# Optimization experiments

Measured on AMD Instinct MI355X. Metric: run time of the kernel, lower is better.

## Reference

```python
import jax, jax.numpy as jnp
import numpy as np

HID = 64
NUM_LAYER = 3
N_OBJ = 100000
N_P1, N_P2, N_P3 = 200000, 400000, 200000
NUM_GRAPHS = 256


def _mlp(x, w1, b1, w2, b2):
    # pyg.nn.MLP([in, hid, out], norm=None): Linear -> ReLU -> Linear
    return jnp.dot(jax.nn.relu(jnp.dot(x, w1) + b1), w2) + b2


def _gather(obj, ei):
    # ei: [arity, n_atoms] object index per argument slot
    r, n = ei.shape
    g = jnp.take(obj, ei, axis=0)  # [r, n, HID]
    return jnp.moveaxis(g, 0, 1).reshape(n, r * HID)  # concat per-position embeddings


def _scatter(atom, ei, n_obj):
    # split atom embedding [n, r*HID] into r chunks and scatter-add to objects
    r, n = ei.shape
    chunks = jnp.moveaxis(atom.reshape(n, r, HID), 1, 0).reshape(r * n, HID)
    return jax.ops.segment_sum(chunks, ei.reshape(-1), num_segments=n_obj)


def _lin_init(key, fan_in, fan_out):
    kw, kb = jax.random.split(key)
    w = jax.random.normal(kw, (fan_in, fan_out), jnp.float32) / np.float32(np.sqrt(fan_in))
    b = jax.random.normal(kb, (fan_out,), jnp.float32) * 0.01
    return w, b


def setup_inputs() -> dict:
    key = jax.random.key(0)
    ks = jax.random.split(key, 16)
    inp = {}
    inp["x_obj"] = jnp.zeros((N_OBJ, 1), jnp.float32)
    inp["x_p1"] = jnp.zeros((N_P1, 1), jnp.float32)
    inp["x_p2"] = jnp.zeros((N_P2, 2), jnp.float32)
    inp["x_p3"] = jnp.zeros((N_P3, 3), jnp.float32)
    for i, (name, r) in enumerate([("p1", 1), ("p2", 2), ("p3", 3)]):
        d = HID * r
        w1, b1 = _lin_init(ks[2 * i], d, d)
        w2, b2 = _lin_init(ks[2 * i + 1], d, d)
        inp[f"w_{name}_1"], inp[f"b_{name}_1"] = w1, b1
        inp[f"w_{name}_2"], inp[f"b_{name}_2"] = w2, b2
    inp["w_u1"], inp["b_u1"] = _lin_init(ks[6], 2 * HID, 2 * HID)
    inp["w_u2"], inp["b_u2"] = _lin_init(ks[7], 2 * HID, HID)
    inp["w_r1"], inp["b_r1"] = _lin_init(ks[8], HID, 2 * HID)
    inp["w_r2"], inp["b_r2"] = _lin_init(ks[9], 2 * HID, 1)
    inp["ei_p1"] = jax.random.randint(ks[10], (1, N_P1), 0, N_OBJ, jnp.int32)
    inp["ei_p2"] = jax.random.randint(ks[11], (2, N_P2), 0, N_OBJ, jnp.int32)
    inp["ei_p3"] = jax.random.randint(ks[12], (3, N_P3), 0, N_OBJ, jnp.int32)
    inp["batch_obj"] = jnp.sort(jax.random.randint(ks[13], (N_OBJ,), 0, NUM_GRAPHS, jnp.int32))
    inp["num_graphs"] = NUM_GRAPHS
    return inp


def reference(x_obj, x_p1, x_p2, x_p3,
              w_p1_1, b_p1_1, w_p1_2, b_p1_2,
              w_p2_1, b_p2_1, w_p2_2, b_p2_2,
              w_p3_1, b_p3_1, w_p3_2, b_p3_2,
              w_u1, b_u1, w_u2, b_u2,
              w_r1, b_r1, w_r2, b_r2,
              ei_p1, ei_p2, ei_p3, batch_obj, num_graphs):
    n_obj = x_obj.shape[0]
    # encoding_layer: everything starts at zeros of size [N, F*hidden]
    obj = jnp.zeros((n_obj, x_obj.shape[1] * HID), jnp.float32)
    for _ in range(NUM_LAYER):
        # FanOutMP: gather arg-object embeddings, per-predicate MLP -> atom embeddings
        a1 = _mlp(_gather(obj, ei_p1), w_p1_1, b_p1_1, w_p1_2, b_p1_2)
        a2 = _mlp(_gather(obj, ei_p2), w_p2_1, b_p2_1, w_p2_2, b_p2_2)
        a3 = _mlp(_gather(obj, ei_p3), w_p3_1, b_p3_1, w_p3_2, b_p3_2)
        # FanInMP: split atom emb into arity chunks, scatter-add back to objects
        agg = (_scatter(a1, ei_p1, n_obj) + _scatter(a2, ei_p2, n_obj)
               + _scatter(a3, ei_p3, n_obj))
        # obj_update on cat([old_obj, aggregated])
        obj = _mlp(jnp.concatenate([obj, agg], axis=1), w_u1, b_u1, w_u2, b_u2)
    # global_add_pool + readout
    pooled = jax.ops.segment_sum(obj, batch_obj, num_segments=num_graphs)
    return _mlp(pooled, w_r1, b_r1, w_r2, b_r2).reshape(-1)
```

## Files before the change

### kernel.cpp

```cpp
#include <hip/hip_runtime.h>
#include <hip/hip_fp16.h>

typedef _Float16 h8 __attribute__((ext_vector_type(8)));
typedef float f32x4 __attribute__((ext_vector_type(4)));

__device__ __forceinline__ f32x4 mfma2(h8 ah, h8 bh, h8 bl, f32x4 c) {
    c = __builtin_amdgcn_mfma_f32_16x16x32_f16(ah, bh, c, 0, 0, 0);
    c = __builtin_amdgcn_mfma_f32_16x16x32_f16(ah, bl, c, 0, 0, 0);
    return c;
}

__launch_bounds__(256)
__global__ void setup_k(const float* __restrict__ w_p1_1, const float* __restrict__ w_p1_2,
                        const float* __restrict__ w_p2_1, const float* __restrict__ w_p2_2,
                        const float* __restrict__ w_p3_1, const float* __restrict__ w_p3_2,
                        const float* __restrict__ w_u1, const float* __restrict__ w_u2,
                        _Float16* __restrict__ hb,
                        const float* __restrict__ b_p1_1, const float* __restrict__ b_p1_2,
                        const float* __restrict__ b_p2_1, const float* __restrict__ b_p2_2,
                        const float* __restrict__ b_p3_1, const float* __restrict__ b_p3_2,
                        float* __restrict__ ac,
                        const int* __restrict__ ei1, const int* __restrict__ ei2,
                        const int* __restrict__ ei3, int* __restrict__ counts,
                        int n_obj, int n1, int n2, int n3)
{
    int b = blockIdx.x;
    if (b < 544) {
        const float* src; int K, N, base; size_t off;
        if      (b < 16)  { src = w_p1_1; K = 64;  N = 64;  base = 0;   off = 0;      }
        else if (b < 32)  { src = w_p1_2; K = 64;  N = 64;  base = 16;  off = 8192;   }
        else if (b < 96)  { src = w_p2_1; K = 128; N = 128; base = 32;  off = 16384;  }
        else if (b < 160) { src = w_p2_2; K = 128; N = 128; base = 96;  off = 49152;  }
        else if (b < 304) { src = w_p3_1; K = 192; N = 192; base = 160; off = 81920;  }
        else if (b < 448) { src = w_p3_2; K = 192; N = 192; base = 304; off = 155648; }
        else if (b < 512) { src = w_u1;   K = 128; N = 128; base = 448; off = 229376; }
        else              { src = w_u2;   K = 128; N = 64;  base = 512; off = 262144; }
        int e = (b - base) * 256 + threadIdx.x;
        if (e < K * N) {
            int n = e / K, k = e - n * K;
            float x = src[k * N + n];
            _Float16 h = (_Float16)x;
            hb[off + e] = h;
            hb[off + (size_t)K * N + e] = (_Float16)(x - (float)h);
        }
    } else if (b < 547) {
        int p = b - 544;
        const float *b1, *w2, *b2; int D, off;
        if      (p == 0) { b1 = b_p1_1; w2 = w_p1_2; b2 = b_p1_2; D = 64;  off = 0;   }
        else if (p == 1) { b1 = b_p2_1; w2 = w_p2_2; b2 = b_p2_2; D = 128; off = 64;  }
        else             { b1 = b_p3_1; w2 = w_p3_2; b2 = b_p3_2; D = 192; off = 192; }
        int n = threadIdx.x;
        if (n < D) {
            float s = b2[n];
            for (int k = 0; k < D; ++k) {
                float h = b1[k];
                h = h > 0.f ? h : 0.f;
                s = fmaf(h, w2[k * D + n], s);
            }
            ac[off + n] = s;
        }
    } else {
        int e = (b - 547) * 256 + threadIdx.x;
        int t1 = n1, t2 = n1 + 2 * n2, t3 = t2 + 3 * n3;
        int o, j;
        if (e < t1) { o = ei1[e]; j = 0; }
        else if (e < t2) { int x = e - t1; o = ei2[x]; j = 1 + (x >= n2 ? 1 : 0); }
        else if (e < t3) { int y = e - t2; o = ei3[y]; j = 3 + (y >= n3 ? 1 : 0) + (y >= 2 * n3 ? 1 : 0); }
        else return;
        atomicAdd(&counts[(size_t)j * n_obj + o], 1);
        atomicAdd(&counts[(size_t)6 * n_obj + o], 1);
    }
}

__launch_bounds__(256)
__global__ void scan1_k(const int* __restrict__ deg, int* __restrict__ rowptr,
                        int* __restrict__ bsum, int n)
{
    __shared__ int buf[256];
    int tid = threadIdx.x;
    int base = blockIdx.x * 1024 + tid * 4;
    int v[4];
#pragma unroll
    for (int k = 0; k < 4; ++k) { int i = base + k; v[k] = (i < n) ? deg[i] : 0; }
    int tsum = v[0] + v[1] + v[2] + v[3];
    buf[tid] = tsum;
    __syncthreads();
    for (int off = 1; off < 256; off <<= 1) {
        int t = (tid >= off) ? buf[tid - off] : 0;
        __syncthreads();
        buf[tid] += t;
        __syncthreads();
    }
    int run = buf[tid] - tsum;
#pragma unroll
    for (int k = 0; k < 4; ++k) {
        int i = base + k;
        if (i < n) rowptr[i] = run;
        run += v[k];
    }
    if (tid == 255) bsum[blockIdx.x] = buf[255];
}

__launch_bounds__(256)
__global__ void scan2_k(int* __restrict__ bsum, int* __restrict__ rowptr, int n, int nb)
{
    __shared__ int buf[256];
    int tid = threadIdx.x;
    int v = (tid < nb) ? bsum[tid] : 0;
    buf[tid] = v;
    __syncthreads();
    for (int off = 1; off < 256; off <<= 1) {
        int t = (tid >= off) ? buf[tid - off] : 0;
        __syncthreads();
        buf[tid] += t;
        __syncthreads();
    }
    if (tid < nb) bsum[tid] = buf[tid] - v;
    if (tid == 255) rowptr[n] = buf[255];
}

__launch_bounds__(256)
__global__ void scan3_k(int* __restrict__ rowptr, int* __restrict__ cursor,
                        const int* __restrict__ bsum, int n)
{
    int i = blockIdx.x * 256 + threadIdx.x;
    if (i < n) {
        int r = rowptr[i] + bsum[i >> 10];
        rowptr[i] = r;
        cursor[i] = r;
    }
}

__launch_bounds__(256)
__global__ void fill_k(const int* __restrict__ ei1, const int* __restrict__ ei2,
                       const int* __restrict__ ei3, int* __restrict__ cursor,
                       int* __restrict__ epos, int n1, int n2, int n3)
{
    int e = blockIdx.x * 256 + threadIdx.x;
    int t1 = n1, t2 = n1 + 2 * n2, t3 = t2 + 3 * n3;
    int o;
    if (e < t1) o = ei1[e];
    else if (e < t2) o = ei2[e - t1];
    else if (e < t3) o = ei3[e - t2];
    else return;
    epos[e] = atomicAdd(&cursor[o], 1);
}

__launch_bounds__(256)
__global__ void bcast_k(const int* __restrict__ counts, const float* __restrict__ ac,
                        _Float16* __restrict__ aggh, int n_obj)
{
    __shared__ float ch[384];
    int tid = threadIdx.x;
    for (int i = tid; i < 384; i += 256) ch[i] = ac[i];
    __syncthreads();
    int i = blockIdx.x * 256 + tid;
    int o = i >> 3, q = i & 7;
    if (o < n_obj) {
        float c[6];
#pragma unroll
        for (int j = 0; j < 6; ++j) c[j] = (float)counts[(size_t)j * n_obj + o];
        h8 v;
#pragma unroll
        for (int comp = 0; comp < 8; ++comp) {
            int col = 8 * q + comp;
            float s = 0.f;
#pragma unroll
            for (int j = 0; j < 6; ++j) s = fmaf(c[j], ch[j * 64 + col], s);
            v[comp] = (_Float16)s;
        }
        *(h8*)(aggh + (size_t)o * 64 + 8 * q) = v;
    }
}

__device__ __forceinline__ void update_tail(
    _Float16* __restrict__ Ah, _Float16* __restrict__ objh,
    const _Float16* __restrict__ W1h, const _Float16* __restrict__ W1l,
    const float* __restrict__ B1,
    const _Float16* __restrict__ W2h, const _Float16* __restrict__ W2l,
    const float* __restrict__ B2,
    int n_obj, int a_base, int last, float* __restrict__ aggf)
{
    constexpr int LDA = 136;
    const int tid = threadIdx.x;
    const int wave = tid >> 6, lane = tid & 63;
    const int r = lane & 15, g = lane >> 4;

    f32x4 z = {0.f, 0.f, 0.f, 0.f};
    f32x4 acc[4][2];
#pragma unroll
    for (int rt = 0; rt < 4; ++rt) { acc[rt][0] = z; acc[rt][1] = z; }
    {
        h8 bh[2][2], bl[2][2];
#pragma unroll
        for (int t = 0; t < 2; ++t) {
            size_t wo = (size_t)((wave * 2 + t) * 16 + r) * 128 + g * 8;
            bh[0][t] = *(const h8*)(W1h + wo);
            bl[0][t] = *(const h8*)(W1l + wo);
        }
#pragma unroll
        for (int kc = 0; kc < 4; ++kc) {
            const int cur = kc & 1, nxt = cur ^ 1;
            if (kc + 1 < 4) {
#pragma unroll
                for (int t = 0; t < 2; ++t) {
                    size_t wo = (size_t)((wave * 2 + t) * 16 + r) * 128 + (kc + 1) * 32 + g * 8;
                    bh[nxt][t] = *(const h8*)(W1h + wo);
                    bl[nxt][t] = *(const h8*)(W1l + wo);
                }
            }
            const int ko = kc * 32 + g * 8;
            h8 ah[4];
#pragma unroll
            for (int rt = 0; rt < 4; ++rt)
                ah[rt] = *(const h8*)(Ah + (rt * 16 + r) * LDA + ko);
#pragma unroll
            for (int t = 0; t < 2; ++t)
#pragma unroll
                for (int rt = 0; rt < 4; ++rt)
                    acc[rt][t] = mfma2(ah[rt], bh[cur][t], bl[cur][t], acc[rt][t]);
        }
    }
    __syncthreads();
#pragma unroll
    for (int t = 0; t < 2; ++t) {
        int col = (wave * 2 + t) * 16 + r;
        float b1 = B1[col];
#pragma unroll
        for (int rt = 0; rt < 4; ++rt)
#pragma unroll
            for (int q = 0; q < 4; ++q) {
                int row = rt * 16 + g * 4 + q;
                float h = acc[rt][t][q] + b1;
                h = h > 0.f ? h : 0.f;
                Ah[row * LDA + col] = (_Float16)h;
            }
    }
    __syncthreads();

    f32x4 acc2[4];
#pragma unroll
    for (int rt = 0; rt < 4; ++rt) acc2[rt] = z;
    {
        h8 bh[2], bl[2];
        {
            size_t wo = (size_t)(wave * 16 + r) * 128 + g * 8;
            bh[0] = *(const h8*)(W2h + wo);
            bl[0] = *(const h8*)(W2l + wo);
        }
#pragma unroll
        for (int kc = 0; kc < 4; ++kc) {
            const int cur = kc & 1, nxt = cur ^ 1;
            if (kc + 1 < 4) {
                size_t wo = (size_t)(wave * 16 + r) * 128 + (kc + 1) * 32 + g * 8;
                bh[nxt] = *(const h8*)(W2h + wo);
                bl[nxt] = *(const h8*)(W2l + wo);
            }
            const int ko = kc * 32 + g * 8;
#pragma unroll
            for (int rt = 0; rt < 4; ++rt) {
                h8 ah = *(const h8*)(Ah + (rt * 16 + r) * LDA + ko);
                acc2[rt] = mfma2(ah, bh[cur], bl[cur], acc2[rt]);
            }
        }
    }
    {
        int col = wave * 16 + r;
        float b2 = B2[col];
#pragma unroll
        for (int rt = 0; rt < 4; ++rt)
#pragma unroll
            for (int q = 0; q < 4; ++q) {
                int row = a_base + rt * 16 + g * 4 + q;
                if (row < n_obj) {
                    float v = acc2[rt][q] + b2;
                    if (last) aggf[(size_t)row * 64 + col] = v;
                    else objh[(size_t)row * 64 + col] = (_Float16)v;
                }
            }
    }
}

__launch_bounds__(256, 4)
__global__ void update0_bcast(_Float16* __restrict__ objh,
                              const int* __restrict__ counts, const float* __restrict__ ac,
                              const _Float16* __restrict__ W1h, const _Float16* __restrict__ W1l,
                              const float* __restrict__ B1,
                              const _Float16* __restrict__ W2h, const _Float16* __restrict__ W2l,
                              const float* __restrict__ B2, int n_obj)
{
    constexpr int LDA = 136;
    __shared__ _Float16 Ah[64 * LDA];
    __shared__ float ch[384];
    const int tid = threadIdx.x;
    const int a_base = blockIdx.x * 64;

    for (int i = tid; i < 384; i += 256) ch[i] = ac[i];
    __syncthreads();
#pragma unroll
    for (int i = 0; i < 4; ++i) {
        int f = tid + 256 * i;
        int a = f >> 4, c = f & 15;
        int rg = a_base + a; if (rg >= n_obj) rg = n_obj - 1;
        h8 v;
        if (c < 8) {
            v = (h8)(_Float16)0.f;
        } else {
            float cc[6];
#pragma unroll
            for (int j = 0; j < 6; ++j) cc[j] = (float)counts[(size_t)j * n_obj + rg];
#pragma unroll
            for (int comp = 0; comp < 8; ++comp) {
                int col = (c - 8) * 8 + comp;
                float s = 0.f;
#pragma unroll
                for (int j = 0; j < 6; ++j) s = fmaf(cc[j], ch[j * 64 + col], s);
                v[comp] = (_Float16)s;
            }
        }
        *(h8*)(Ah + a * LDA + c * 8) = v;
    }
    __syncthreads();
    update_tail(Ah, objh, W1h, W1l, B1, W2h, W2l, B2, n_obj, a_base, 0, nullptr);
}

template<int FIRST>
__launch_bounds__(256, 4)
__global__ void update_mfma(_Float16* __restrict__ objh, _Float16* __restrict__ aggh,
                            const _Float16* __restrict__ W1h, const _Float16* __restrict__ W1l,
                            const float* __restrict__ B1,
                            const _Float16* __restrict__ W2h, const _Float16* __restrict__ W2l,
                            const float* __restrict__ B2,
                            int n_obj, int zero_agg, int last, float* __restrict__ aggf)
{
    constexpr int LDA = 136;
    __shared__ _Float16 Ah[64 * LDA];
    const int tid = threadIdx.x;
    const int a_base = blockIdx.x * 64;
#pragma unroll
    for (int i = 0; i < 4; ++i) {
        int f = tid + 256 * i;
        int a = f >> 4, c = f & 15;
        int rg = a_base + a; if (rg >= n_obj) rg = n_obj - 1;
        h8 v;
        if (c < 8) {
            if (FIRST) v = (h8)(_Float16)0.f;
            else v = *(const h8*)(objh + (size_t)rg * 64 + c * 8);
        } else {
            v = *(const h8*)(aggh + (size_t)rg * 64 + (c - 8) * 8);
        }
        *(h8*)(Ah + a * LDA + c * 8) = v;
    }
    __syncthreads();
    update_tail(Ah, objh, W1h, W1l, B1, W2h, W2l, B2, n_obj, a_base, last, aggf);
    if (zero_agg) {
        __syncthreads();
        h8 zz = (h8)(_Float16)0.f;
#pragma unroll
        for (int i = 0; i < 2; ++i) {
            int f = tid + 256 * i;
            int a = f >> 3, q = f & 7;
            int rg = a_base + a;
            if (rg < n_obj) *(h8*)(aggh + (size_t)rg * 64 + q * 8) = zz;
        }
    }
}

template<int R, int STORE>
__device__ __forceinline__ void pred_body(
    char* smem,
    const _Float16* __restrict__ objh, const int* __restrict__ ei,
    const int* __restrict__ epos, int cbase,
    const _Float16* __restrict__ W1h, const _Float16* __restrict__ W1l,
    const float* __restrict__ B1,
    const _Float16* __restrict__ W2h, const _Float16* __restrict__ W2l,
    const float* __restrict__ B2,
    _Float16* __restrict__ aggh, _Float16* __restrict__ chunks,
    int n_atoms, int blk)
{
    constexpr int D = 64 * R;
    constexpr int KC = D / 32;
    constexpr int LDA = D + 8;
    _Float16* Ah = (_Float16*)smem;
    int* eis = (int*)(Ah + 64 * LDA);

    const int tid = threadIdx.x;
    const int wave = tid >> 6, lane = tid & 63;
    const int r = lane & 15, g = lane >> 4;
    const int a_base = blk * 64;
    const int tb = wave * R;

    for (int i = tid; i < R * 64; i += 256) {
        int s = i >> 6, a = i & 63;
        int ag = a_base + a; if (ag >= n_atoms) ag = n_atoms - 1;
        eis[i] = ei[s * n_atoms + ag];
    }
    __syncthreads();
    {
        h8 vv[2 * R];
#pragma unroll
        for (int i = 0; i < 2 * R; ++i) {
            int f = tid + 256 * i;
            int rowslot = f >> 3, c = f & 7;
            int s = rowslot >> 6, a = rowslot & 63;
            vv[i] = *(const h8*)(objh + (size_t)eis[s * 64 + a] * 64 + c * 8);
        }
#pragma unroll
        for (int i = 0; i < 2 * R; ++i) {
            int f = tid + 256 * i;
            int rowslot = f >> 3, c = f & 7;
            int s = rowslot >> 6, a = rowslot & 63;
            *(h8*)(Ah + a * LDA + s * 64 + c * 8) = vv[i];
        }
    }
    __syncthreads();

    f32x4 z = {0.f, 0.f, 0.f, 0.f};
    f32x4 acc[4][R];
#pragma unroll
    for (int rt = 0; rt < 4; ++rt)
#pragma unroll
        for (int t = 0; t < R; ++t) acc[rt][t] = z;

    {
        h8 bh[2][R], bl[2][R];
#pragma unroll
        for (int t = 0; t < R; ++t) {
            size_t wo = (size_t)((tb + t) * 16 + r) * D + g * 8;
            bh[0][t] = *(const h8*)(W1h + wo);
            bl[0][t] = *(const h8*)(W1l + wo);
        }
#pragma unroll
        for (int kc = 0; kc < KC; ++kc) {
            const int cur = kc & 1, nxt = cur ^ 1;
            if (kc + 1 < KC) {
#pragma unroll
                for (int t = 0; t < R; ++t) {
                    size_t wo = (size_t)((tb + t) * 16 + r) * D + (kc + 1) * 32 + g * 8;
                    bh[nxt][t] = *(const h8*)(W1h + wo);
                    bl[nxt][t] = *(const h8*)(W1l + wo);
                }
            }
            const int ko = kc * 32 + g * 8;
            h8 ah[4];
#pragma unroll
            for (int rt = 0; rt < 4; ++rt)
                ah[rt] = *(const h8*)(Ah + (rt * 16 + r) * LDA + ko);
#pragma unroll
            for (int t = 0; t < R; ++t)
#pragma unroll
                for (int rt = 0; rt < 4; ++rt)
                    acc[rt][t] = mfma2(ah[rt], bh[cur][t], bl[cur][t], acc[rt][t]);
        }
    }
    __syncthreads();
#pragma unroll
    for (int t = 0; t < R; ++t) {
        int col = (tb + t) * 16 + r;
        float b1 = B1[col];
#pragma unroll
        for (int rt = 0; rt < 4; ++rt)
#pragma unroll
            for (int q = 0; q < 4; ++q) {
                int row = rt * 16 + g * 4 + q;
                float h = acc[rt][t][q] + b1;
                h = h > 0.f ? h : 0.f;
                Ah[row * LDA + col] = (_Float16)h;
            }
    }
    __syncthreads();

#pragma unroll
    for (int rt = 0; rt < 4; ++rt)
#pragma unroll
        for (int t = 0; t < R; ++t) acc[rt][t] = z;
    {
        h8 bh[2][R], bl[2][R];
#pragma unroll
        for (int t = 0; t < R; ++t) {
            size_t wo = (size_t)((tb + t) * 16 + r) * D + g * 8;
            bh[0][t] = *(const h8*)(W2h + wo);
            bl[0][t] = *(const h8*)(W2l + wo);
        }
#pragma unroll
        for (int kc = 0; kc < KC; ++kc) {
            const int cur = kc & 1, nxt = cur ^ 1;
            if (kc + 1 < KC) {
#pragma unroll
                for (int t = 0; t < R; ++t) {
                    size_t wo = (size_t)((tb + t) * 16 + r) * D + (kc + 1) * 32 + g * 8;
                    bh[nxt][t] = *(const h8*)(W2h + wo);
                    bl[nxt][t] = *(const h8*)(W2l + wo);
                }
            }
            const int ko = kc * 32 + g * 8;
            h8 ah[4];
#pragma unroll
            for (int rt = 0; rt < 4; ++rt)
                ah[rt] = *(const h8*)(Ah + (rt * 16 + r) * LDA + ko);
#pragma unroll
            for (int t = 0; t < R; ++t)
#pragma unroll
                for (int rt = 0; rt < 4; ++rt)
                    acc[rt][t] = mfma2(ah[rt], bh[cur][t], bl[cur][t], acc[rt][t]);
        }
    }

    if (STORE) {
        __syncthreads();
#pragma unroll
        for (int t = 0; t < R; ++t) {
            int col = (tb + t) * 16 + r;
            float b2 = B2[col];
            int s = col >> 6, cc = col & 63;
#pragma unroll
            for (int rt = 0; rt < 4; ++rt)
#pragma unroll
                for (int q = 0; q < 4; ++q) {
                    int row = rt * 16 + g * 4 + q;
                    Ah[row * LDA + s * 64 + cc] = (_Float16)(acc[rt][t][q] + b2);
                }
        }
        __syncthreads();
#pragma unroll
        for (int p = 0; p < 2 * R; ++p) {
            int i = p * 32 + (tid >> 3);
            int s = i >> 6, a = i & 63;
            int c8 = tid & 7;
            int atom = a_base + a;
            if (atom < n_atoms) {
                int pos = epos[cbase + s * n_atoms + atom];
                *(h8*)(chunks + (size_t)pos * 64 + c8 * 8) =
                    *(const h8*)(Ah + a * LDA + s * 64 + c8 * 8);
            }
        }
    } else {
#pragma unroll
        for (int t = 0; t < R; ++t) {
            int col = (tb + t) * 16 + r;
            float b2 = B2[col];
            int s = col >> 6, cc = col & 63;
#pragma unroll
            for (int rt = 0; rt < 4; ++rt)
#pragma unroll
                for (int q = 0; q < 4; ++q) {
                    int row = rt * 16 + g * 4 + q;
                    int atom = a_base + row;
                    float v = acc[rt][t][q] + b2;
                    float v2 = __shfl_xor(v, 1);
                    if (atom < n_atoms && (r & 1) == 0) {
                        __half2 hv = __floats2half2_rn(v, v2);
                        unsafeAtomicAdd((__half2*)(aggh + (size_t)eis[s * 64 + row] * 64 + cc), hv);
                    }
                }
        }
    }
}

template<int STORE>
__launch_bounds__(256, 6)
__global__ void pred_all(const _Float16* __restrict__ objh, _Float16* __restrict__ aggh,
                         _Float16* __restrict__ chunks, const int* __restrict__ epos,
                         const int* __restrict__ ei1, const int* __restrict__ ei2,
                         const int* __restrict__ ei3,
                         const _Float16* __restrict__ hb,
                         const float* __restrict__ b_p1_1, const float* __restrict__ b_p1_2,
                         const float* __restrict__ b_p2_1, const float* __restrict__ b_p2_2,
                         const float* __restrict__ b_p3_1, const float* __restrict__ b_p3_2,
                         int n1, int n2, int n3, int nb3, int nb2)
{
    extern __shared__ char smem[];
    int b = blockIdx.x;
    if (b < nb3) {
        pred_body<3, STORE>(smem, objh, ei3, epos, n1 + 2 * n2,
                            hb + 81920, hb + 118784, b_p3_1,
                            hb + 155648, hb + 192512, b_p3_2, aggh, chunks, n3, b);
    } else if (b < nb3 + nb2) {
        pred_body<2, STORE>(smem, objh, ei2, epos, n1,
                            hb + 16384, hb + 32768, b_p2_1,
                            hb + 49152, hb + 65536, b_p2_2, aggh, chunks, n2, b - nb3);
    } else {
        pred_body<1, STORE>(smem, objh, ei1, epos, 0,
                            hb + 0, hb + 4096, b_p1_1,
                            hb + 8192, hb + 12288, b_p1_2, aggh, chunks, n1, b - nb3 - nb2);
    }
}

__launch_bounds__(256, 4)
__global__ void fanin_update(_Float16* __restrict__ objh,
                             const _Float16* __restrict__ chunks,
                             const int* __restrict__ rowptr,
                             const _Float16* __restrict__ W1h, const _Float16* __restrict__ W1l,
                             const float* __restrict__ B1,
                             const _Float16* __restrict__ W2h, const _Float16* __restrict__ W2l,
                             const float* __restrict__ B2,
                             int n_obj, int last, float* __restrict__ aggf)
{
    constexpr int LDA = 136;
    __shared__ _Float16 Ah[64 * LDA];

    const int tid = threadIdx.x;
    const int a_base = blockIdx.x * 64;

    const int o_local = tid >> 2, part = tid & 3;
    const int o = a_base + o_local;
    const bool valid = o < n_obj;
    const int b = valid ? rowptr[o] : 0;
    const int e2 = valid ? rowptr[o + 1] : 0;
    float s[16];
#pragma unroll
    for (int j = 0; j < 16; ++j) s[j] = 0.f;
    int i = b;
    for (; i + 2 <= e2; i += 2) {
        const h8* c0 = (const h8*)(chunks + (size_t)i * 64 + part * 16);
        const h8* c1 = (const h8*)(chunks + (size_t)(i + 1) * 64 + part * 16);
        h8 a0 = c0[0], a1 = c0[1], d0 = c1[0], d1 = c1[1];
#pragma unroll
        for (int j = 0; j < 8; ++j) {
            s[j] += (float)a0[j] + (float)d0[j];
            s[8 + j] += (float)a1[j] + (float)d1[j];
        }
    }
    if (i < e2) {
        const h8* c0 = (const h8*)(chunks + (size_t)i * 64 + part * 16);
        h8 a0 = c0[0], a1 = c0[1];
#pragma unroll
        for (int j = 0; j < 8; ++j) { s[j] += (float)a0[j]; s[8 + j] += (float)a1[j]; }
    }
    {
        int oc = valid ? o : n_obj - 1;
        h8 u0 = *(const h8*)(objh + (size_t)oc * 64 + part * 16);
        h8 u1 = *(const h8*)(objh + (size_t)oc * 64 + part * 16 + 8);
        *(h8*)(Ah + o_local * LDA + part * 16) = u0;
        *(h8*)(Ah + o_local * LDA + part * 16 + 8) = u1;
        h8 a0, a1;
#pragma unroll
        for (int j = 0; j < 8; ++j) { a0[j] = (_Float16)s[j]; a1[j] = (_Float16)s[8 + j]; }
        *(h8*)(Ah + o_local * LDA + 64 + part * 16) = a0;
        *(h8*)(Ah + o_local * LDA + 64 + part * 16 + 8) = a1;
    }
    __syncthreads();
    update_tail(Ah, objh, W1h, W1l, B1, W2h, W2l, B2, n_obj, a_base, last, aggf);
}

__global__ void pool_kernel(const float* __restrict__ obj, const int* __restrict__ batch,
                            float* __restrict__ pooled, int n_obj)
{
    int i = blockIdx.x * 256 + threadIdx.x;
    int row = i >> 4, q = i & 15;
    if (row < n_obj) {
        float4 v = ((const float4*)obj)[(size_t)row * 16 + q];
        int g = batch[row];
        float* p = pooled + g * 64 + 4 * q;
        atomicAdd(p + 0, v.x);
        atomicAdd(p + 1, v.y);
        atomicAdd(p + 2, v.z);
        atomicAdd(p + 3, v.w);
    }
}

__launch_bounds__(128)
__global__ void readout_kernel(const float* __restrict__ pooled,
                               const float* __restrict__ w1, const float* __restrict__ b1,
                               const float* __restrict__ w2, const float* __restrict__ b2,
                               float* __restrict__ out)
{
    int g = blockIdx.x, c = threadIdx.x;
    __shared__ float xs[64];
    __shared__ float red[2];
    if (c < 64) xs[c] = pooled[g * 64 + c];
    __syncthreads();
    float h = b1[c];
#pragma unroll
    for (int k = 0; k < 64; ++k) h = fmaf(xs[k], w1[k * 128 + c], h);
    float v = fmaxf(h, 0.f) * w2[c];
#pragma unroll
    for (int off = 32; off > 0; off >>= 1) v += __shfl_down(v, off);
    if ((c & 63) == 0) red[c >> 6] = v;
    __syncthreads();
    if (c == 0) out[g] = red[0] + red[1] + b2[0];
}

static inline size_t align_up(size_t x) { return (x + 255) & ~(size_t)255; }

extern "C" void kernel_launch(void* const* d_in, const int* in_sizes, int n_in,
                              void* d_out, int out_size, void* d_ws, size_t ws_size,
                              hipStream_t stream)
{
    const float* w_p1_1 = (const float*)d_in[4];
    const float* b_p1_1 = (const float*)d_in[5];
    const float* w_p1_2 = (const float*)d_in[6];
    const float* b_p1_2 = (const float*)d_in[7];
    const float* w_p2_1 = (const float*)d_in[8];
    const float* b_p2_1 = (const float*)d_in[9];
    const float* w_p2_2 = (const float*)d_in[10];
    const float* b_p2_2 = (const float*)d_in[11];
    const float* w_p3_1 = (const float*)d_in[12];
    const float* b_p3_1 = (const float*)d_in[13];
    const float* w_p3_2 = (const float*)d_in[14];
    const float* b_p3_2 = (const float*)d_in[15];
    const float* w_u1 = (const float*)d_in[16];
    const float* b_u1 = (const float*)d_in[17];
    const float* w_u2 = (const float*)d_in[18];
    const float* b_u2 = (const float*)d_in[19];
    const float* w_r1 = (const float*)d_in[20];
    const float* b_r1 = (const float*)d_in[21];
    const float* w_r2 = (const float*)d_in[22];
    const float* b_r2 = (const float*)d_in[23];
    const int* ei_p1 = (const int*)d_in[24];
    const int* ei_p2 = (const int*)d_in[25];
    const int* ei_p3 = (const int*)d_in[26];
    const int* batch = (const int*)d_in[27];

    const int n_obj = in_sizes[0];
    const int n_p1 = in_sizes[24];
    const int n_p2 = in_sizes[25] / 2;
    const int n_p3 = in_sizes[26] / 3;
    const int E = n_p1 + 2 * n_p2 + 3 * n_p3;

    char* base = (char*)d_ws;
    size_t off = 0;
    _Float16* objh = (_Float16*)(base + off); off = align_up(off + (size_t)n_obj * 64 * 2);
    _Float16* aggh = (_Float16*)(base + off); off = align_up(off + (size_t)n_obj * 64 * 2);
    float* aggf = (float*)(base + off);       off = align_up(off + (size_t)n_obj * 64 * 4);
    float* pooled = (float*)(base + off);     off = align_up(off + (size_t)out_size * 64 * 4);
    _Float16* hb = (_Float16*)(base + off);   off = align_up(off + (size_t)278528 * 2);
    int* counts = (int*)(base + off);         off = align_up(off + (size_t)7 * n_obj * 4);
    int* deg = counts + (size_t)6 * n_obj;
    int* rowptr = (int*)(base + off);         off = align_up(off + ((size_t)n_obj + 1) * 4);
    int* cursor = (int*)(base + off);         off = align_up(off + (size_t)n_obj * 4);
    int* bsum = (int*)(base + off);           off = align_up(off + 256 * 4);
    int* epos = (int*)(base + off);           off = align_up(off + (size_t)E * 4);
    _Float16* chunks = (_Float16*)(base + off); off = align_up(off + (size_t)E * 64 * 2);
    const bool csr_ok = off <= ws_size;
    float* ac = pooled;

    const int nb3 = (n_p3 + 63) / 64, nb2 = (n_p2 + 63) / 64, nb1 = (n_p1 + 63) / 64;
    const int pred_smem = 64 * (192 + 8) * 2 + 3 * 64 * 4;
    const int nbs = (n_obj + 1023) / 1024;

    hipMemsetAsync(counts, 0, (size_t)7 * n_obj * sizeof(int), stream);
    setup_k<<<547 + (E + 255) / 256, 256, 0, stream>>>(
        w_p1_1, w_p1_2, w_p2_1, w_p2_2, w_p3_1, w_p3_2, w_u1, w_u2, hb,
        b_p1_1, b_p1_2, b_p2_1, b_p2_2, b_p3_1, b_p3_2, ac,
        ei_p1, ei_p2, ei_p3, counts, n_obj, n_p1, n_p2, n_p3);
    if (csr_ok) {
        scan1_k<<<nbs, 256, 0, stream>>>(deg, rowptr, bsum, n_obj);
        scan2_k<<<1, 256, 0, stream>>>(bsum, rowptr, n_obj, nbs);
        scan3_k<<<(n_obj + 255) / 256, 256, 0, stream>>>(rowptr, cursor, bsum, n_obj);
        fill_k<<<(E + 255) / 256, 256, 0, stream>>>(ei_p1, ei_p2, ei_p3, cursor, epos,
                                                    n_p1, n_p2, n_p3);
        update0_bcast<<<(n_obj + 63) / 64, 256, 0, stream>>>(
            objh, counts, ac, hb + 229376, hb + 245760, b_u1,
            hb + 262144, hb + 270336, b_u2, n_obj);
        for (int l = 1; l < 3; ++l) {
            pred_all<1><<<nb3 + nb2 + nb1, 256, pred_smem, stream>>>(
                objh, aggh, chunks, epos, ei_p1, ei_p2, ei_p3, hb,
                b_p1_1, b_p1_2, b_p2_1, b_p2_2, b_p3_1, b_p3_2,
                n_p1, n_p2, n_p3, nb3, nb2);
            fanin_update<<<(n_obj + 63) / 64, 256, 0, stream>>>(
                objh, chunks, rowptr,
                hb + 229376, hb + 245760, b_u1, hb + 262144, hb + 270336, b_u2,
                n_obj, l == 2 ? 1 : 0, aggf);
        }
    } else {
        bcast_k<<<((size_t)n_obj * 8 + 255) / 256, 256, 0, stream>>>(counts, ac, aggh, n_obj);
        update_mfma<1><<<(n_obj + 63) / 64, 256, 0, stream>>>(
            objh, aggh, hb + 229376, hb + 245760, b_u1, hb + 262144, hb + 270336, b_u2,
            n_obj, 1, 0, aggf);
        for (int l = 1; l < 3; ++l) {
            pred_all<0><<<nb3 + nb2 + nb1, 256, pred_smem, stream>>>(
                objh, aggh, chunks, epos, ei_p1, ei_p2, ei_p3, hb,
                b_p1_1, b_p1_2, b_p2_1, b_p2_2, b_p3_1, b_p3_2,
                n_p1, n_p2, n_p3, nb3, nb2);
            update_mfma<0><<<(n_obj + 63) / 64, 256, 0, stream>>>(
                objh, aggh, hb + 229376, hb + 245760, b_u1, hb + 262144, hb + 270336, b_u2,
                n_obj, l < 2 ? 1 : 0, l == 2 ? 1 : 0, aggf);
        }
    }
    hipMemsetAsync(pooled, 0, (size_t)out_size * 64 * sizeof(float), stream);
    pool_kernel<<<((size_t)n_obj * 16 + 255) / 256, 256, 0, stream>>>(aggf, batch, pooled, n_obj);
    readout_kernel<<<out_size, 128, 0, stream>>>(pooled, w_r1, b_r1, w_r2, b_r2, (float*)d_out);
}
```

Baseline: 1.303 ms.

## Store chunks in edge order and gather via CSR column indices in fan-in

```diff
diff --git a/kernel.cpp b/kernel.cpp
--- a/kernel.cpp
+++ b/kernel.cpp
@@ -134,7 +134,7 @@
 __launch_bounds__(256)
 __global__ void fill_k(const int* __restrict__ ei1, const int* __restrict__ ei2,
                        const int* __restrict__ ei3, int* __restrict__ cursor,
-                       int* __restrict__ epos, int n1, int n2, int n3)
+                       int* __restrict__ colidx, int n1, int n2, int n3)
 {
     int e = blockIdx.x * 256 + threadIdx.x;
     int t1 = n1, t2 = n1 + 2 * n2, t3 = t2 + 3 * n3;
@@ -143,7 +143,8 @@
     else if (e < t2) o = ei2[e - t1];
     else if (e < t3) o = ei3[e - t2];
     else return;
-    epos[e] = atomicAdd(&cursor[o], 1);
+    int pos = atomicAdd(&cursor[o], 1);
+    colidx[pos] = e;
 }
 
 __launch_bounds__(256)
@@ -369,8 +370,7 @@
 template<int R, int STORE>
 __device__ __forceinline__ void pred_body(
     char* smem,
-    const _Float16* __restrict__ objh, const int* __restrict__ ei,
-    const int* __restrict__ epos, int cbase,
+    const _Float16* __restrict__ objh, const int* __restrict__ ei, int cbase,
     const _Float16* __restrict__ W1h, const _Float16* __restrict__ W1l,
     const float* __restrict__ B1,
     const _Float16* __restrict__ W2h, const _Float16* __restrict__ W2l,
@@ -529,8 +529,8 @@
             int c8 = tid & 7;
             int atom = a_base + a;
             if (atom < n_atoms) {
-                int pos = epos[cbase + s * n_atoms + atom];
-                *(h8*)(chunks + (size_t)pos * 64 + c8 * 8) =
+                size_t pos = (size_t)cbase + (size_t)s * n_atoms + atom;
+                *(h8*)(chunks + pos * 64 + c8 * 8) =
                     *(const h8*)(Ah + a * LDA + s * 64 + c8 * 8);
             }
         }
@@ -560,7 +560,7 @@
 template<int STORE>
 __launch_bounds__(256, 6)
 __global__ void pred_all(const _Float16* __restrict__ objh, _Float16* __restrict__ aggh,
-                         _Float16* __restrict__ chunks, const int* __restrict__ epos,
+                         _Float16* __restrict__ chunks,
                          const int* __restrict__ ei1, const int* __restrict__ ei2,
                          const int* __restrict__ ei3,
                          const _Float16* __restrict__ hb,
@@ -572,15 +572,15 @@
     extern __shared__ char smem[];
     int b = blockIdx.x;
     if (b < nb3) {
-        pred_body<3, STORE>(smem, objh, ei3, epos, n1 + 2 * n2,
+        pred_body<3, STORE>(smem, objh, ei3, n1 + 2 * n2,
                             hb + 81920, hb + 118784, b_p3_1,
                             hb + 155648, hb + 192512, b_p3_2, aggh, chunks, n3, b);
     } else if (b < nb3 + nb2) {
-        pred_body<2, STORE>(smem, objh, ei2, epos, n1,
+        pred_body<2, STORE>(smem, objh, ei2, n1,
                             hb + 16384, hb + 32768, b_p2_1,
                             hb + 49152, hb + 65536, b_p2_2, aggh, chunks, n2, b - nb3);
     } else {
-        pred_body<1, STORE>(smem, objh, ei1, epos, 0,
+        pred_body<1, STORE>(smem, objh, ei1, 0,
                             hb + 0, hb + 4096, b_p1_1,
                             hb + 8192, hb + 12288, b_p1_2, aggh, chunks, n1, b - nb3 - nb2);
     }
@@ -589,7 +589,7 @@
 __launch_bounds__(256, 4)
 __global__ void fanin_update(_Float16* __restrict__ objh,
                              const _Float16* __restrict__ chunks,
-                             const int* __restrict__ rowptr,
+                             const int* __restrict__ rowptr, const int* __restrict__ colidx,
                              const _Float16* __restrict__ W1h, const _Float16* __restrict__ W1l,
                              const float* __restrict__ B1,
                              const _Float16* __restrict__ W2h, const _Float16* __restrict__ W2l,
@@ -598,9 +598,17 @@
 {
     constexpr int LDA = 136;
     __shared__ _Float16 Ah[64 * LDA];
+    __shared__ int cidx[2048];
 
     const int tid = threadIdx.x;
     const int a_base = blockIdx.x * 64;
+    const int o_hi = (a_base + 64 < n_obj) ? a_base + 64 : n_obj;
+
+    const int sbeg = rowptr[a_base];
+    const int send = rowptr[o_hi];
+    const int total = send - sbeg;
+    const int ncache = total < 2048 ? total : 2048;
+    for (int i = tid; i < ncache; i += 256) cidx[i] = colidx[sbeg + i];
 
     const int o_local = tid >> 2, part = tid & 3;
     const int o = a_base + o_local;
@@ -610,10 +618,14 @@
     float s[16];
 #pragma unroll
     for (int j = 0; j < 16; ++j) s[j] = 0.f;
+    __syncthreads();
     int i = b;
     for (; i + 2 <= e2; i += 2) {
-        const h8* c0 = (const h8*)(chunks + (size_t)i * 64 + part * 16);
-        const h8* c1 = (const h8*)(chunks + (size_t)(i + 1) * 64 + part * 16);
+        int li0 = i - sbeg, li1 = li0 + 1;
+        int r0 = (li0 < ncache) ? cidx[li0] : colidx[i];
+        int r1 = (li1 < ncache) ? cidx[li1] : colidx[i + 1];
+        const h8* c0 = (const h8*)(chunks + (size_t)r0 * 64 + part * 16);
+        const h8* c1 = (const h8*)(chunks + (size_t)r1 * 64 + part * 16);
         h8 a0 = c0[0], a1 = c0[1], d0 = c1[0], d1 = c1[1];
 #pragma unroll
         for (int j = 0; j < 8; ++j) {
@@ -622,7 +634,9 @@
         }
     }
     if (i < e2) {
-        const h8* c0 = (const h8*)(chunks + (size_t)i * 64 + part * 16);
+        int li0 = i - sbeg;
+        int r0 = (li0 < ncache) ? cidx[li0] : colidx[i];
+        const h8* c0 = (const h8*)(chunks + (size_t)r0 * 64 + part * 16);
         h8 a0 = c0[0], a1 = c0[1];
 #pragma unroll
         for (int j = 0; j < 8; ++j) { s[j] += (float)a0[j]; s[8 + j] += (float)a1[j]; }
@@ -730,7 +744,7 @@
     int* rowptr = (int*)(base + off);         off = align_up(off + ((size_t)n_obj + 1) * 4);
     int* cursor = (int*)(base + off);         off = align_up(off + (size_t)n_obj * 4);
     int* bsum = (int*)(base + off);           off = align_up(off + 256 * 4);
-    int* epos = (int*)(base + off);           off = align_up(off + (size_t)E * 4);
+    int* colidx = (int*)(base + off);         off = align_up(off + (size_t)E * 4);
     _Float16* chunks = (_Float16*)(base + off); off = align_up(off + (size_t)E * 64 * 2);
     const bool csr_ok = off <= ws_size;
     float* ac = pooled;
@@ -748,18 +762,18 @@
         scan1_k<<<nbs, 256, 0, stream>>>(deg, rowptr, bsum, n_obj);
         scan2_k<<<1, 256, 0, stream>>>(bsum, rowptr, n_obj, nbs);
         scan3_k<<<(n_obj + 255) / 256, 256, 0, stream>>>(rowptr, cursor, bsum, n_obj);
-        fill_k<<<(E + 255) / 256, 256, 0, stream>>>(ei_p1, ei_p2, ei_p3, cursor, epos,
+        fill_k<<<(E + 255) / 256, 256, 0, stream>>>(ei_p1, ei_p2, ei_p3, cursor, colidx,
                                                     n_p1, n_p2, n_p3);
         update0_bcast<<<(n_obj + 63) / 64, 256, 0, stream>>>(
             objh, counts, ac, hb + 229376, hb + 245760, b_u1,
             hb + 262144, hb + 270336, b_u2, n_obj);
         for (int l = 1; l < 3; ++l) {
             pred_all<1><<<nb3 + nb2 + nb1, 256, pred_smem, stream>>>(
-                objh, aggh, chunks, epos, ei_p1, ei_p2, ei_p3, hb,
+                objh, aggh, chunks, ei_p1, ei_p2, ei_p3, hb,
                 b_p1_1, b_p1_2, b_p2_1, b_p2_2, b_p3_1, b_p3_2,
                 n_p1, n_p2, n_p3, nb3, nb2);
             fanin_update<<<(n_obj + 63) / 64, 256, 0, stream>>>(
-                objh, chunks, rowptr,
+                objh, chunks, rowptr, colidx,
                 hb + 229376, hb + 245760, b_u1, hb + 262144, hb + 270336, b_u2,
                 n_obj, l == 2 ? 1 : 0, aggf);
         }
@@ -770,7 +784,7 @@
             n_obj, 1, 0, aggf);
         for (int l = 1; l < 3; ++l) {
             pred_all<0><<<nb3 + nb2 + nb1, 256, pred_smem, stream>>>(
-                objh, aggh, chunks, epos, ei_p1, ei_p2, ei_p3, hb,
+                objh, aggh, chunks, ei_p1, ei_p2, ei_p3, hb,
                 b_p1_1, b_p1_2, b_p2_1, b_p2_2, b_p3_1, b_p3_2,
                 n_p1, n_p2, n_p3, nb3, nb2);
             update_mfma<0><<<(n_obj + 63) / 64, 256, 0, stream>>>(
```

After: 1.347 ms. 1.03x slower.

## Load-balance CSR fan-in reduction across threads with segmented LDS atomic accumulation

Applied to the files above, without the earlier changes.

```diff
diff --git a/kernel.cpp b/kernel.cpp
--- a/kernel.cpp
+++ b/kernel.cpp
@@ -143,7 +143,8 @@
     else if (e < t2) o = ei2[e - t1];
     else if (e < t3) o = ei3[e - t2];
     else return;
-    epos[e] = atomicAdd(&cursor[o], 1);
+    int pos = atomicAdd(&cursor[o], 1);
+    epos[e] = pos;
 }
 
 __launch_bounds__(256)
@@ -598,46 +599,68 @@
 {
     constexpr int LDA = 136;
     __shared__ _Float16 Ah[64 * LDA];
+    __shared__ float accf[64 * 68];
+    __shared__ int rowptrS[65];
 
     const int tid = threadIdx.x;
     const int a_base = blockIdx.x * 64;
 
-    const int o_local = tid >> 2, part = tid & 3;
-    const int o = a_base + o_local;
-    const bool valid = o < n_obj;
-    const int b = valid ? rowptr[o] : 0;
-    const int e2 = valid ? rowptr[o + 1] : 0;
-    float s[16];
-#pragma unroll
-    for (int j = 0; j < 16; ++j) s[j] = 0.f;
-    int i = b;
-    for (; i + 2 <= e2; i += 2) {
-        const h8* c0 = (const h8*)(chunks + (size_t)i * 64 + part * 16);
-        const h8* c1 = (const h8*)(chunks + (size_t)(i + 1) * 64 + part * 16);
-        h8 a0 = c0[0], a1 = c0[1], d0 = c1[0], d1 = c1[1];
-#pragma unroll
-        for (int j = 0; j < 8; ++j) {
-            s[j] += (float)a0[j] + (float)d0[j];
-            s[8 + j] += (float)a1[j] + (float)d1[j];
-        }
-    }
-    if (i < e2) {
-        const h8* c0 = (const h8*)(chunks + (size_t)i * 64 + part * 16);
-        h8 a0 = c0[0], a1 = c0[1];
-#pragma unroll
-        for (int j = 0; j < 8; ++j) { s[j] += (float)a0[j]; s[8 + j] += (float)a1[j]; }
-    }
-    {
-        int oc = valid ? o : n_obj - 1;
-        h8 u0 = *(const h8*)(objh + (size_t)oc * 64 + part * 16);
-        h8 u1 = *(const h8*)(objh + (size_t)oc * 64 + part * 16 + 8);
-        *(h8*)(Ah + o_local * LDA + part * 16) = u0;
-        *(h8*)(Ah + o_local * LDA + part * 16 + 8) = u1;
-        h8 a0, a1;
-#pragma unroll
-        for (int j = 0; j < 8; ++j) { a0[j] = (_Float16)s[j]; a1[j] = (_Float16)s[8 + j]; }
-        *(h8*)(Ah + o_local * LDA + 64 + part * 16) = a0;
-        *(h8*)(Ah + o_local * LDA + 64 + part * 16 + 8) = a1;
+    if (tid < 65) {
+        int idx = a_base + tid;
+        rowptrS[tid] = rowptr[idx <= n_obj ? idx : n_obj];
+    }
+    for (int i = tid; i < 64 * 68; i += 256) accf[i] = 0.f;
+    __syncthreads();
+
+    const int sbeg = rowptrS[0];
+    const int send = rowptrS[64];
+    const int total = send - sbeg;
+    const int grp = tid >> 3, c8 = tid & 7;
+    const int len = (total + 31) >> 5;
+    const int beg = sbeg + grp * len;
+    const int end = (beg + len < send) ? beg + len : send;
+
+    if (beg < end) {
+        int lo = 0;
+#pragma unroll
+        for (int st = 32; st > 0; st >>= 1) {
+            int cand = lo + st;
+            if (cand <= 63 && rowptrS[cand] <= beg) lo = cand;
+        }
+        int o_local = lo;
+        float loc[8];
+#pragma unroll
+        for (int j = 0; j < 8; ++j) loc[j] = 0.f;
+        for (int row = beg; row < end; ++row) {
+            if (row >= rowptrS[o_local + 1]) {
+#pragma unroll
+                for (int j = 0; j < 8; ++j)
+                    atomicAdd(&accf[o_local * 68 + c8 * 8 + j], loc[j]);
+#pragma unroll
+                for (int j = 0; j < 8; ++j) loc[j] = 0.f;
+                do { ++o_local; } while (row >= rowptrS[o_local + 1]);
+            }
+            h8 v = *(const h8*)(chunks + (size_t)row * 64 + c8 * 8);
+#pragma unroll
+            for (int j = 0; j < 8; ++j) loc[j] += (float)v[j];
+        }
+#pragma unroll
+        for (int j = 0; j < 8; ++j)
+            atomicAdd(&accf[o_local * 68 + c8 * 8 + j], loc[j]);
+    }
+    __syncthreads();
+
+#pragma unroll
+    for (int i = 0; i < 2; ++i) {
+        int f = tid + 256 * i;
+        int a = f >> 3, c = f & 7;
+        int rg = a_base + a; if (rg >= n_obj) rg = n_obj - 1;
+        h8 u = *(const h8*)(objh + (size_t)rg * 64 + c * 8);
+        *(h8*)(Ah + a * LDA + c * 8) = u;
+        h8 w;
+#pragma unroll
+        for (int j = 0; j < 8; ++j) w[j] = (_Float16)accf[a * 68 + c * 8 + j];
+        *(h8*)(Ah + a * LDA + 64 + c * 8) = w;
     }
     __syncthreads();
     update_tail(Ah, objh, W1h, W1l, B1, W2h, W2l, B2, n_obj, a_base, last, aggf);
```

After: 1.367 ms. +4.9%, slower.
